# Optimization experiments

Hardware: AMD Instinct MI355X
Metric: run time of the kernel (lower is better)

Reference implementation:

```python
import jax, jax.numpy as jnp
import numpy as np

B, IN, H = 8192, 1024, 1024


def setup_inputs() -> dict:
    key = jax.random.key(0)
    kx, kh, kc, kwx, kwh = jax.random.split(key, 5)
    return {
        "x": jax.random.normal(kx, (B, IN), dtype=jnp.float32),
        "h": jax.random.normal(kh, (B, H), dtype=jnp.float32),
        "c": jax.random.normal(kc, (B, H), dtype=jnp.float32),
        # 8 Dense layers fused: gate order [i, f, g, o] along last axis
        "Wx": jax.random.normal(kwx, (IN, 4 * H), dtype=jnp.float32) * 0.02,
        "Wh": jax.random.normal(kwh, (H, 4 * H), dtype=jnp.float32) * 0.02,
        "bx": jnp.zeros((4 * H,), dtype=jnp.float32),
        "bh": jnp.zeros((4 * H,), dtype=jnp.float32),
    }


def reference(x, h, c, Wx, Wh, bx, bh):
    # Fused equivalent of the 8 separate Dense layers:
    #   gate_k = x @ Wx[:, k] + bx[k] + h @ Wh[:, k] + bh[k]
    gates = x @ Wx + h @ Wh + (bx + bh)  # [B, 4H]
    i, f, g, o = jnp.split(gates, 4, axis=-1)
    i = jax.nn.sigmoid(i)
    f = jax.nn.sigmoid(f)
    g = jnp.tanh(g)
    o = jax.nn.sigmoid(o)
    c_new = f * c + i * g
    h_new = o * jnp.tanh(c_new)
    # Original returns (out_gate, hidden_state, cell_state)
    return (o, h_new, c_new)
```

## Files before the change

### kernel.cpp

```cpp
#include <hip/hip_runtime.h>
#include <hip/hip_bf16.h>

typedef __attribute__((ext_vector_type(8))) short bf16x8;
typedef __attribute__((ext_vector_type(4))) float f32x4;
typedef __attribute__((ext_vector_type(8))) unsigned short u16x8;

#define B_DIM 8192
#define H_DIM 1024
#define K_DIM 2048
#define N_DIM 4096
#define BH (B_DIM * H_DIM)

__device__ __forceinline__ unsigned short f2bf(float f) {
    union { float f; unsigned u; } v; v.f = f;
    unsigned r = v.u + 0x7FFFu + ((v.u >> 16) & 1u);
    return (unsigned short)(r >> 16);
}

__device__ __forceinline__ void gload16(const void* g, void* l) {
    __builtin_amdgcn_global_load_lds(
        (const __attribute__((address_space(1))) void*)g,
        (__attribute__((address_space(3))) void*)l, 16, 0, 0);
}

__global__ void prep(const float* __restrict__ x, const float* __restrict__ h,
                     const float* __restrict__ Wx, const float* __restrict__ Wh,
                     unsigned short* __restrict__ Abf, unsigned short* __restrict__ Bperm) {
    __shared__ float tile[64][65];
    const int t = threadIdx.x;
    if (blockIdx.x < 8192) {
        int gid = blockIdx.x * 256 + t;
        size_t e = (size_t)gid * 8;
        int m   = gid >> 8;
        int col = (gid & 255) * 8;
        int p   = col >> 10;
        int k   = col & 1023;
        const float* src = (p ? h : x) + (size_t)m * 1024 + k;
        float4 v0 = *(const float4*)src;
        float4 v1 = *(const float4*)(src + 4);
        u16x8 o = { f2bf(v0.x), f2bf(v0.y), f2bf(v0.z), f2bf(v0.w),
                    f2bf(v1.x), f2bf(v1.y), f2bf(v1.z), f2bf(v1.w) };
        *(u16x8*)(Abf + e) = o;
        return;
    }
    const int bz = blockIdx.x - 8192;
    const int k0 = (bz & 31) * 64;
    const int n0 = (bz >> 5) * 64;
#pragma unroll
    for (int it = 0; it < 4; ++it) {
        int lin = it * 256 + t;
        int kl  = lin >> 4;
        int n4  = lin & 15;
        int k   = k0 + kl;
        const float* src = (k < 1024) ? (Wx + (size_t)k * 4096 + n0 + n4 * 4)
                                      : (Wh + (size_t)(k - 1024) * 4096 + n0 + n4 * 4);
        float4 v = *(const float4*)src;
        tile[kl][n4 * 4 + 0] = v.x;
        tile[kl][n4 * 4 + 1] = v.y;
        tile[kl][n4 * 4 + 2] = v.z;
        tile[kl][n4 * 4 + 3] = v.w;
    }
    __syncthreads();
#pragma unroll
    for (int it = 0; it < 2; ++it) {
        int lin = it * 256 + t;
        int nl  = lin >> 3;
        int ch  = lin & 7;
        int n    = n0 + nl;
        int gate = n >> 10;
        int j    = n & 1023;
        int jb   = j >> 5;
        int jj   = j & 31;
        int R    = jb * 128 + (jj >> 4) * 64 + gate * 16 + (jj & 15);
        u16x8 o;
#pragma unroll
        for (int q = 0; q < 8; ++q) o[q] = f2bf(tile[ch * 8 + q][nl]);
        *(u16x8*)(Bperm + (size_t)R * 2048 + k0 + ch * 8) = o;
    }
}

__global__ __launch_bounds__(256, 4) void lstm_fused(
    const unsigned short* __restrict__ Abf,
    const unsigned short* __restrict__ Bperm,
    const float* __restrict__ bx, const float* __restrict__ bh,
    const float* __restrict__ cin, float* __restrict__ out) {
    __shared__ unsigned short lsA[128 * 64];
    __shared__ unsigned short lsB[128 * 64];

    const int tid  = threadIdx.x;
    const int wave = tid >> 6;
    const int lane = tid & 63;
    const int m0 = blockIdx.x * 128;
    const int jb = blockIdx.y;
    const int wm = wave >> 1;
    const int wn = wave & 1;

    f32x4 acc[4][4];
#pragma unroll
    for (int i = 0; i < 4; ++i)
#pragma unroll
        for (int j = 0; j < 4; ++j) acc[i][j] = (f32x4){0.f, 0.f, 0.f, 0.f};

    const int sRow   = tid >> 3;
    const int sChunk = (((tid & 7) ^ ((tid >> 3) & 7))) * 8;
    const int aBase = (m0 + sRow) * K_DIM + sChunk;
    const int bBase = (jb * 128 + sRow) * K_DIM + sChunk;

    const int fRow  = lane & 15;
    const int qBase = lane >> 4;
    const int rx    = fRow & 7;

    for (int kt = 0; kt < 32; ++kt) {
        const int kOff = kt * 64;
#pragma unroll
        for (int it = 0; it < 4; ++it) {
            gload16(Abf + aBase + it * (32 * K_DIM) + kOff, lsA + it * 2048 + wave * 512);
            gload16(Bperm + bBase + it * (32 * K_DIM) + kOff, lsB + it * 2048 + wave * 512);
        }
        __syncthreads();
#pragma unroll
        for (int ks = 0; ks < 2; ++ks) {
            bf16x8 af[4], bfr[4];
            const int qPhys = (ks * 4 + qBase) ^ rx;
#pragma unroll
            for (int tm = 0; tm < 4; ++tm)
                af[tm] = *(const bf16x8*)(lsA + (wm * 64 + tm * 16 + fRow) * 64 + qPhys * 8);
#pragma unroll
            for (int tn = 0; tn < 4; ++tn)
                bfr[tn] = *(const bf16x8*)(lsB + (wn * 64 + tn * 16 + fRow) * 64 + qPhys * 8);
#pragma unroll
            for (int tm = 0; tm < 4; ++tm)
#pragma unroll
                for (int tn = 0; tn < 4; ++tn)
                    acc[tm][tn] = __builtin_amdgcn_mfma_f32_16x16x32_bf16(
                        af[tm], bfr[tn], acc[tm][tn], 0, 0, 0);
        }
        __syncthreads();
    }

    const int j = jb * 32 + wn * 16 + fRow;
    const float b_i = bx[j] + bh[j];
    const float b_f = bx[1024 + j] + bh[1024 + j];
    const float b_g = bx[2048 + j] + bh[2048 + j];
    const float b_o = bx[3072 + j] + bh[3072 + j];
#pragma unroll
    for (int tm = 0; tm < 4; ++tm) {
#pragma unroll
        for (int r = 0; r < 4; ++r) {
            const int row = m0 + wm * 64 + tm * 16 + (lane >> 4) * 4 + r;
            float vi = acc[tm][0][r] + b_i;
            float vf = acc[tm][1][r] + b_f;
            float vg = acc[tm][2][r] + b_g;
            float vo = acc[tm][3][r] + b_o;
            float ig = 1.f / (1.f + __expf(-vi));
            float fg = 1.f / (1.f + __expf(-vf));
            float e2g = __expf(2.f * fminf(fmaxf(vg, -15.f), 15.f));
            float gg = (e2g - 1.f) / (e2g + 1.f);
            float og = 1.f / (1.f + __expf(-vo));
            float cn = fg * cin[(size_t)row * 1024 + j] + ig * gg;
            float e2c = __expf(2.f * fminf(fmaxf(cn, -15.f), 15.f));
            float hn = og * ((e2c - 1.f) / (e2c + 1.f));
            out[(size_t)row * 1024 + j] = og;
            out[(size_t)BH + (size_t)row * 1024 + j] = hn;
            out[(size_t)2 * BH + (size_t)row * 1024 + j] = cn;
        }
    }
}

extern "C" void kernel_launch(void* const* d_in, const int* in_sizes, int n_in,
                              void* d_out, int out_size, void* d_ws, size_t ws_size,
                              hipStream_t stream) {
    const float* x  = (const float*)d_in[0];
    const float* h  = (const float*)d_in[1];
    const float* c  = (const float*)d_in[2];
    const float* Wx = (const float*)d_in[3];
    const float* Wh = (const float*)d_in[4];
    const float* bx = (const float*)d_in[5];
    const float* bh = (const float*)d_in[6];
    float* out = (float*)d_out;

    unsigned short* Abf   = (unsigned short*)d_ws;
    unsigned short* Bperm = (unsigned short*)((char*)d_ws + (size_t)B_DIM * K_DIM * 2);

    hipLaunchKernelGGL(prep, dim3(8192 + 2048), dim3(256), 0, stream, x, h, Wx, Wh, Abf, Bperm);
    hipLaunchKernelGGL(lstm_fused, dim3(B_DIM / 128, 32), dim3(256), 0, stream,
                       Abf, Bperm, bx, bh, c, out);
}
```

Before: 340.2 us.

## Load B fragments directly to registers from prepacked layout, bypassing LDS

The weight matrix is now prepacked into an MFMA-fragment-ordered layout so each lane can load its B operands straight from global memory into registers. These loads are double-buffered one k-tile ahead, and the B shared-memory tile is removed. The single prep kernel is split into separate A and B conversion kernels, with the A pass handling 16 elements per thread. This cuts LDS traffic and B staging, but adds register pressure (launch bounds lowered to 3 blocks per CU) and makes B loads uncached in LDS across waves, so global and L2 traffic for B rises.

```diff
diff --git a/kernel.cpp b/kernel.cpp
--- a/kernel.cpp
+++ b/kernel.cpp
@@ -23,29 +23,32 @@
         (__attribute__((address_space(3))) void*)l, 16, 0, 0);
 }
 
-__global__ void prep(const float* __restrict__ x, const float* __restrict__ h,
-                     const float* __restrict__ Wx, const float* __restrict__ Wh,
-                     unsigned short* __restrict__ Abf, unsigned short* __restrict__ Bperm) {
+__global__ void prep_a(const float* __restrict__ x, const float* __restrict__ h,
+                       unsigned short* __restrict__ Abf) {
+    int gid = blockIdx.x * 256 + threadIdx.x;
+    size_t e = (size_t)gid * 16;
+    int m   = gid >> 7;
+    int col = (gid & 127) * 16;
+    const float* src = (col >= 1024) ? (h + (size_t)m * 1024 + col - 1024)
+                                     : (x + (size_t)m * 1024 + col);
+    float4 v0 = *(const float4*)(src + 0);
+    float4 v1 = *(const float4*)(src + 4);
+    float4 v2 = *(const float4*)(src + 8);
+    float4 v3 = *(const float4*)(src + 12);
+    u16x8 o0 = { f2bf(v0.x), f2bf(v0.y), f2bf(v0.z), f2bf(v0.w),
+                 f2bf(v1.x), f2bf(v1.y), f2bf(v1.z), f2bf(v1.w) };
+    u16x8 o1 = { f2bf(v2.x), f2bf(v2.y), f2bf(v2.z), f2bf(v2.w),
+                 f2bf(v3.x), f2bf(v3.y), f2bf(v3.z), f2bf(v3.w) };
+    *(u16x8*)(Abf + e)     = o0;
+    *(u16x8*)(Abf + e + 8) = o1;
+}
+
+__global__ void prep_b(const float* __restrict__ Wx, const float* __restrict__ Wh,
+                       unsigned short* __restrict__ Bpack) {
     __shared__ float tile[64][65];
-    const int t = threadIdx.x;
-    if (blockIdx.x < 8192) {
-        int gid = blockIdx.x * 256 + t;
-        size_t e = (size_t)gid * 8;
-        int m   = gid >> 8;
-        int col = (gid & 255) * 8;
-        int p   = col >> 10;
-        int k   = col & 1023;
-        const float* src = (p ? h : x) + (size_t)m * 1024 + k;
-        float4 v0 = *(const float4*)src;
-        float4 v1 = *(const float4*)(src + 4);
-        u16x8 o = { f2bf(v0.x), f2bf(v0.y), f2bf(v0.z), f2bf(v0.w),
-                    f2bf(v1.x), f2bf(v1.y), f2bf(v1.z), f2bf(v1.w) };
-        *(u16x8*)(Abf + e) = o;
-        return;
-    }
-    const int bz = blockIdx.x - 8192;
-    const int k0 = (bz & 31) * 64;
-    const int n0 = (bz >> 5) * 64;
+    const int t  = threadIdx.x;
+    const int k0 = (blockIdx.x & 31) * 64;
+    const int n0 = (blockIdx.x >> 5) * 64;
 #pragma unroll
     for (int it = 0; it < 4; ++it) {
         int lin = it * 256 + t;
@@ -70,22 +73,26 @@
         int gate = n >> 10;
         int j    = n & 1023;
         int jb   = j >> 5;
-        int jj   = j & 31;
-        int R    = jb * 128 + (jj >> 4) * 64 + gate * 16 + (jj & 15);
+        int wn   = (j >> 4) & 1;
+        int fR   = j & 15;
+        int kt   = k0 >> 6;
+        int ks   = ch >> 2;
+        int qB   = ch & 3;
+        size_t off = (size_t)jb * 262144 + wn * 131072 + kt * 4096 + ks * 2048
+                   + gate * 512 + (qB * 16 + fR) * 8;
         u16x8 o;
 #pragma unroll
         for (int q = 0; q < 8; ++q) o[q] = f2bf(tile[ch * 8 + q][nl]);
-        *(u16x8*)(Bperm + (size_t)R * 2048 + k0 + ch * 8) = o;
-    }
-}
-
-__global__ __launch_bounds__(256, 4) void lstm_fused(
+        *(u16x8*)(Bpack + off) = o;
+    }
+}
+
+__global__ __launch_bounds__(256, 3) void lstm_fused(
     const unsigned short* __restrict__ Abf,
-    const unsigned short* __restrict__ Bperm,
+    const unsigned short* __restrict__ Bpack,
     const float* __restrict__ bx, const float* __restrict__ bh,
     const float* __restrict__ cin, float* __restrict__ out) {
     __shared__ unsigned short lsA[128 * 64];
-    __shared__ unsigned short lsB[128 * 64];
 
     const int tid  = threadIdx.x;
     const int wave = tid >> 6;
@@ -103,37 +110,49 @@
 
     const int sRow   = tid >> 3;
     const int sChunk = (((tid & 7) ^ ((tid >> 3) & 7))) * 8;
-    const int aBase = (m0 + sRow) * K_DIM + sChunk;
-    const int bBase = (jb * 128 + sRow) * K_DIM + sChunk;
+    const int aBase  = (m0 + sRow) * K_DIM + sChunk;
 
     const int fRow  = lane & 15;
     const int qBase = lane >> 4;
     const int rx    = fRow & 7;
 
+    const unsigned short* bPtr = Bpack + (size_t)jb * 262144 + wn * 131072 + lane * 8;
+
+    bf16x8 bbuf[2][8];
+#pragma unroll
+    for (int ks = 0; ks < 2; ++ks)
+#pragma unroll
+        for (int tn = 0; tn < 4; ++tn)
+            bbuf[0][ks * 4 + tn] = *(const bf16x8*)(bPtr + ks * 2048 + tn * 512);
+
+#pragma unroll 2
     for (int kt = 0; kt < 32; ++kt) {
+        const int p = kt & 1;
         const int kOff = kt * 64;
 #pragma unroll
-        for (int it = 0; it < 4; ++it) {
+        for (int it = 0; it < 4; ++it)
             gload16(Abf + aBase + it * (32 * K_DIM) + kOff, lsA + it * 2048 + wave * 512);
-            gload16(Bperm + bBase + it * (32 * K_DIM) + kOff, lsB + it * 2048 + wave * 512);
-        }
+        const int ktn = (kt == 31) ? 31 : kt + 1;
+#pragma unroll
+        for (int ks = 0; ks < 2; ++ks)
+#pragma unroll
+            for (int tn = 0; tn < 4; ++tn)
+                bbuf[p ^ 1][ks * 4 + tn] =
+                    *(const bf16x8*)(bPtr + ktn * 4096 + ks * 2048 + tn * 512);
         __syncthreads();
 #pragma unroll
         for (int ks = 0; ks < 2; ++ks) {
-            bf16x8 af[4], bfr[4];
+            bf16x8 af[4];
             const int qPhys = (ks * 4 + qBase) ^ rx;
 #pragma unroll
             for (int tm = 0; tm < 4; ++tm)
                 af[tm] = *(const bf16x8*)(lsA + (wm * 64 + tm * 16 + fRow) * 64 + qPhys * 8);
 #pragma unroll
-            for (int tn = 0; tn < 4; ++tn)
-                bfr[tn] = *(const bf16x8*)(lsB + (wn * 64 + tn * 16 + fRow) * 64 + qPhys * 8);
-#pragma unroll
             for (int tm = 0; tm < 4; ++tm)
 #pragma unroll
                 for (int tn = 0; tn < 4; ++tn)
                     acc[tm][tn] = __builtin_amdgcn_mfma_f32_16x16x32_bf16(
-                        af[tm], bfr[tn], acc[tm][tn], 0, 0, 0);
+                        af[tm], bbuf[p][ks * 4 + tn], acc[tm][tn], 0, 0, 0);
         }
         __syncthreads();
     }
@@ -147,7 +166,7 @@
     for (int tm = 0; tm < 4; ++tm) {
 #pragma unroll
         for (int r = 0; r < 4; ++r) {
-            const int row = m0 + wm * 64 + tm * 16 + (lane >> 4) * 4 + r;
+            const int row = m0 + wm * 64 + tm * 16 + qBase * 4 + r;
             float vi = acc[tm][0][r] + b_i;
             float vf = acc[tm][1][r] + b_f;
             float vg = acc[tm][2][r] + b_g;
@@ -180,9 +199,10 @@
     float* out = (float*)d_out;
 
     unsigned short* Abf   = (unsigned short*)d_ws;
-    unsigned short* Bperm = (unsigned short*)((char*)d_ws + (size_t)B_DIM * K_DIM * 2);
-
-    hipLaunchKernelGGL(prep, dim3(8192 + 2048), dim3(256), 0, stream, x, h, Wx, Wh, Abf, Bperm);
+    unsigned short* Bpack = (unsigned short*)((char*)d_ws + (size_t)B_DIM * K_DIM * 2);
+
+    hipLaunchKernelGGL(prep_b, dim3(2048), dim3(256), 0, stream, Wx, Wh, Bpack);
+    hipLaunchKernelGGL(prep_a, dim3(4096), dim3(256), 0, stream, x, h, Abf);
     hipLaunchKernelGGL(lstm_fused, dim3(B_DIM / 128, 32), dim3(256), 0, stream,
-                       Abf, Bperm, bx, bh, c, out);
-}
+                       Abf, Bpack, bx, bh, c, out);
+}
```

Result: slower. 349.1 us (+2.6%).

## Switch GEMM to 32x32x16 MFMA with 256-row tiles and relayout weights

Applied to the files above, without the earlier changes.

Replaces the 16x16x32 MFMA tiling with 32x32x16 bf16 MFMA. The block tile grows to 256 rows by 128 permuted columns, and each wave owns 64 rows across all 128 columns. The weight permutation is changed so each 32-column group holds one gate, matching the wider MFMA output. The prep kernel also converts 16 activations per thread instead of 8. The aim is to raise arithmetic intensity per LDS read and reduce how often B tiles are reloaded, at the cost of more LDS (48KB), more accumulator registers, lower occupancy (launch bounds 3), and fewer blocks.

```diff
diff --git a/kernel.cpp b/kernel.cpp
--- a/kernel.cpp
+++ b/kernel.cpp
@@ -2,7 +2,7 @@
 #include <hip/hip_bf16.h>
 
 typedef __attribute__((ext_vector_type(8))) short bf16x8;
-typedef __attribute__((ext_vector_type(4))) float f32x4;
+typedef __attribute__((ext_vector_type(16))) float f32x16;
 typedef __attribute__((ext_vector_type(8))) unsigned short u16x8;
 
 #define B_DIM 8192
@@ -28,22 +28,26 @@
                      unsigned short* __restrict__ Abf, unsigned short* __restrict__ Bperm) {
     __shared__ float tile[64][65];
     const int t = threadIdx.x;
-    if (blockIdx.x < 8192) {
+    if (blockIdx.x < 4096) {
         int gid = blockIdx.x * 256 + t;
-        size_t e = (size_t)gid * 8;
-        int m   = gid >> 8;
-        int col = (gid & 255) * 8;
-        int p   = col >> 10;
-        int k   = col & 1023;
-        const float* src = (p ? h : x) + (size_t)m * 1024 + k;
-        float4 v0 = *(const float4*)src;
+        size_t e = (size_t)gid * 16;
+        int m   = gid >> 7;
+        int col = (gid & 127) * 16;
+        const float* src = (col >= 1024) ? (h + (size_t)m * 1024 + col - 1024)
+                                         : (x + (size_t)m * 1024 + col);
+        float4 v0 = *(const float4*)(src + 0);
         float4 v1 = *(const float4*)(src + 4);
-        u16x8 o = { f2bf(v0.x), f2bf(v0.y), f2bf(v0.z), f2bf(v0.w),
-                    f2bf(v1.x), f2bf(v1.y), f2bf(v1.z), f2bf(v1.w) };
-        *(u16x8*)(Abf + e) = o;
+        float4 v2 = *(const float4*)(src + 8);
+        float4 v3 = *(const float4*)(src + 12);
+        u16x8 o0 = { f2bf(v0.x), f2bf(v0.y), f2bf(v0.z), f2bf(v0.w),
+                     f2bf(v1.x), f2bf(v1.y), f2bf(v1.z), f2bf(v1.w) };
+        u16x8 o1 = { f2bf(v2.x), f2bf(v2.y), f2bf(v2.z), f2bf(v2.w),
+                     f2bf(v3.x), f2bf(v3.y), f2bf(v3.z), f2bf(v3.w) };
+        *(u16x8*)(Abf + e)     = o0;
+        *(u16x8*)(Abf + e + 8) = o1;
         return;
     }
-    const int bz = blockIdx.x - 8192;
+    const int bz = blockIdx.x - 4096;
     const int k0 = (bz & 31) * 64;
     const int n0 = (bz >> 5) * 64;
 #pragma unroll
@@ -69,9 +73,7 @@
         int n    = n0 + nl;
         int gate = n >> 10;
         int j    = n & 1023;
-        int jb   = j >> 5;
-        int jj   = j & 31;
-        int R    = jb * 128 + (jj >> 4) * 64 + gate * 16 + (jj & 15);
+        int R    = (j >> 5) * 128 + gate * 32 + (j & 31);
         u16x8 o;
 #pragma unroll
         for (int q = 0; q < 8; ++q) o[q] = f2bf(tile[ch * 8 + q][nl]);
@@ -79,75 +81,76 @@
     }
 }
 
-__global__ __launch_bounds__(256, 4) void lstm_fused(
+__global__ __launch_bounds__(256, 3) void lstm_fused(
     const unsigned short* __restrict__ Abf,
     const unsigned short* __restrict__ Bperm,
     const float* __restrict__ bx, const float* __restrict__ bh,
     const float* __restrict__ cin, float* __restrict__ out) {
-    __shared__ unsigned short lsA[128 * 64];
+    __shared__ unsigned short lsA[256 * 64];
     __shared__ unsigned short lsB[128 * 64];
 
     const int tid  = threadIdx.x;
     const int wave = tid >> 6;
     const int lane = tid & 63;
-    const int m0 = blockIdx.x * 128;
+    const int m0 = blockIdx.x * 256;
     const int jb = blockIdx.y;
-    const int wm = wave >> 1;
-    const int wn = wave & 1;
 
-    f32x4 acc[4][4];
+    f32x16 acc[2][4];
 #pragma unroll
-    for (int i = 0; i < 4; ++i)
+    for (int tm = 0; tm < 2; ++tm)
 #pragma unroll
-        for (int j = 0; j < 4; ++j) acc[i][j] = (f32x4){0.f, 0.f, 0.f, 0.f};
+        for (int tn = 0; tn < 4; ++tn)
+#pragma unroll
+            for (int r = 0; r < 16; ++r) acc[tm][tn][r] = 0.f;
 
     const int sRow   = tid >> 3;
     const int sChunk = (((tid & 7) ^ ((tid >> 3) & 7))) * 8;
-    const int aBase = (m0 + sRow) * K_DIM + sChunk;
-    const int bBase = (jb * 128 + sRow) * K_DIM + sChunk;
+    const int aBase  = (m0 + sRow) * K_DIM + sChunk;
+    const int bBase  = (jb * 128 + sRow) * K_DIM + sChunk;
 
-    const int fRow  = lane & 15;
-    const int qBase = lane >> 4;
-    const int rx    = fRow & 7;
+    const int col = lane & 31;
+    const int kh  = lane >> 5;
+    const int cx  = lane & 7;
 
     for (int kt = 0; kt < 32; ++kt) {
         const int kOff = kt * 64;
 #pragma unroll
-        for (int it = 0; it < 4; ++it) {
+        for (int it = 0; it < 8; ++it)
             gload16(Abf + aBase + it * (32 * K_DIM) + kOff, lsA + it * 2048 + wave * 512);
+#pragma unroll
+        for (int it = 0; it < 4; ++it)
             gload16(Bperm + bBase + it * (32 * K_DIM) + kOff, lsB + it * 2048 + wave * 512);
-        }
         __syncthreads();
 #pragma unroll
-        for (int ks = 0; ks < 2; ++ks) {
-            bf16x8 af[4], bfr[4];
-            const int qPhys = (ks * 4 + qBase) ^ rx;
+        for (int ks = 0; ks < 4; ++ks) {
+            const int cp = ((ks * 2 + kh) ^ cx) * 8;
+            bf16x8 af[2], bfr[4];
 #pragma unroll
-            for (int tm = 0; tm < 4; ++tm)
-                af[tm] = *(const bf16x8*)(lsA + (wm * 64 + tm * 16 + fRow) * 64 + qPhys * 8);
+            for (int tm = 0; tm < 2; ++tm)
+                af[tm] = *(const bf16x8*)(lsA + (wave * 64 + tm * 32 + col) * 64 + cp);
 #pragma unroll
             for (int tn = 0; tn < 4; ++tn)
-                bfr[tn] = *(const bf16x8*)(lsB + (wn * 64 + tn * 16 + fRow) * 64 + qPhys * 8);
+                bfr[tn] = *(const bf16x8*)(lsB + (tn * 32 + col) * 64 + cp);
 #pragma unroll
-            for (int tm = 0; tm < 4; ++tm)
+            for (int tm = 0; tm < 2; ++tm)
 #pragma unroll
                 for (int tn = 0; tn < 4; ++tn)
-                    acc[tm][tn] = __builtin_amdgcn_mfma_f32_16x16x32_bf16(
+                    acc[tm][tn] = __builtin_amdgcn_mfma_f32_32x32x16_bf16(
                         af[tm], bfr[tn], acc[tm][tn], 0, 0, 0);
         }
         __syncthreads();
     }
 
-    const int j = jb * 32 + wn * 16 + fRow;
+    const int j = jb * 32 + col;
     const float b_i = bx[j] + bh[j];
     const float b_f = bx[1024 + j] + bh[1024 + j];
     const float b_g = bx[2048 + j] + bh[2048 + j];
     const float b_o = bx[3072 + j] + bh[3072 + j];
 #pragma unroll
-    for (int tm = 0; tm < 4; ++tm) {
+    for (int tm = 0; tm < 2; ++tm) {
 #pragma unroll
-        for (int r = 0; r < 4; ++r) {
-            const int row = m0 + wm * 64 + tm * 16 + (lane >> 4) * 4 + r;
+        for (int r = 0; r < 16; ++r) {
+            const int row = m0 + wave * 64 + tm * 32 + (r & 3) + 8 * (r >> 2) + 4 * kh;
             float vi = acc[tm][0][r] + b_i;
             float vf = acc[tm][1][r] + b_f;
             float vg = acc[tm][2][r] + b_g;
@@ -182,7 +185,7 @@
     unsigned short* Abf   = (unsigned short*)d_ws;
     unsigned short* Bperm = (unsigned short*)((char*)d_ws + (size_t)B_DIM * K_DIM * 2);
 
-    hipLaunchKernelGGL(prep, dim3(8192 + 2048), dim3(256), 0, stream, x, h, Wx, Wh, Abf, Bperm);
-    hipLaunchKernelGGL(lstm_fused, dim3(B_DIM / 128, 32), dim3(256), 0, stream,
+    hipLaunchKernelGGL(prep, dim3(4096 + 2048), dim3(256), 0, stream, x, h, Wx, Wh, Abf, Bperm);
+    hipLaunchKernelGGL(lstm_fused, dim3(B_DIM / 256, 32), dim3(256), 0, stream,
                        Abf, Bperm, bx, bh, c, out);
 }
```

After: 374.8 us. 1.1x slower.
